# Kernel tuning notes

Hardware: AMD Instinct MI355X
Metric: run time of the kernel (lower is better)

## Reference

```python
import jax, jax.numpy as jnp
import numpy as np
from math import factorial as fact

L_MAX = 3
K = 128
N = 8192

# ---- Clebsch-Gordan coefficients (Racah formula, real for integer l) ----

def _cg_coeff(l1, m1, l2, m2, l3, m3):
    if m1 + m2 != m3:
        return 0.0
    pref = ((2 * l3 + 1) * fact(l3 + l1 - l2) * fact(l3 - l1 + l2)
            * fact(l1 + l2 - l3) / fact(l1 + l2 + l3 + 1)) ** 0.5
    pref *= (fact(l3 + m3) * fact(l3 - m3) * fact(l1 - m1) * fact(l1 + m1)
             * fact(l2 - m2) * fact(l2 + m2)) ** 0.5
    s = 0.0
    for k in range(max(0, l2 - l3 - m1, l1 - l3 + m2),
                   min(l1 + l2 - l3, l1 - m1, l2 + m2) + 1):
        s += (-1) ** k / (fact(k) * fact(l1 + l2 - l3 - k) * fact(l1 - m1 - k)
                          * fact(l2 + m2 - k) * fact(l3 - l2 + m1 + k)
                          * fact(l3 - l1 - m2 + k))
    return pref * s


def _cg_tensor(l1, l2, l3):
    C = np.zeros((2 * l1 + 1, 2 * l2 + 1, 2 * l3 + 1), dtype=np.float32)
    for m1 in range(-l1, l1 + 1):
        for m2 in range(-l2, l2 + 1):
            m3 = m1 + m2
            if -l3 <= m3 <= l3:
                C[m1 + l1, m2 + l2, m3 + l3] = _cg_coeff(l1, m1, l2, m2, l3, m3)
    return jnp.asarray(C)

# all allowed (l1, l2, l3) coupling paths, deterministic order
PATHS = [(l1, l2, l3)
         for l1 in range(L_MAX + 1)
         for l2 in range(L_MAX + 1)
         for l3 in range(abs(l1 - l2), min(l1 + l2, L_MAX) + 1)]
CG = {p: _cg_tensor(*p) for p in PATHS}
N_PATHS = [sum(1 for p in PATHS if p[2] == l3) for l3 in range(L_MAX + 1)]  # [4,9,11,10]


def setup_inputs() -> dict:
    key = jax.random.key(0)
    ks = jax.random.split(key, 12)
    inp = {}
    for i, l in enumerate(range(L_MAX + 1)):
        inp[f"f1_l{l}"] = jax.random.normal(ks[i], (N, 2 * l + 1, K), jnp.float32)
        inp[f"f2_l{l}"] = jax.random.normal(ks[4 + i], (N, 2 * l + 1, K), jnp.float32)
        fan_in = N_PATHS[l] * K
        inp[f"W_l{l}"] = jax.random.normal(ks[8 + i], (fan_in, K), jnp.float32) / np.sqrt(fan_in)
    return inp


def _forward(f1, f2, W):
    # CG tensor product: per-path contraction, channel-wise in k
    tp = [[] for _ in range(L_MAX + 1)]
    for (l1, l2, l3) in PATHS:
        C = CG[(l1, l2, l3)]  # [2l1+1, 2l2+1, 2l3+1]
        tp[l3].append(jnp.einsum('abm,nak,nbk->nmk', C, f1[l1], f2[l2]))
    # concat paths along channels, linear mix back to K, residual add
    outs = []
    for l3 in range(L_MAX + 1):
        cat = jnp.concatenate(tp[l3], axis=-1)        # [N, 2l3+1, n_paths*K]
        mixed = jnp.einsum('nmp,pk->nmk', cat, W[l3])  # [N, 2l3+1, K]
        outs.append(f1[l3] + mixed)
    return tuple(outs)


def reference(f1_l0, f1_l1, f1_l2, f1_l3,
              f2_l0, f2_l1, f2_l2, f2_l3,
              W_l0, W_l1, W_l2, W_l3):
    f1 = [f1_l0, f1_l1, f1_l2, f1_l3]
    f2 = [f2_l0, f2_l1, f2_l2, f2_l3]
    W = [W_l0, W_l1, W_l2, W_l3]
    return _forward(f1, f2, W)
```

## Files before the change

### kernel.cpp

```cpp
#include <hip/hip_runtime.h>

#define K_DIM 128

typedef __attribute__((ext_vector_type(8))) short short8;
typedef __attribute__((ext_vector_type(4))) float f32x4;

constexpr int C_L1[34] = {0,0,0,0, 1,1,1,1,1,1,1,1,1, 2,2,2,2,2,2,2,2,2,2,2, 3,3,3,3,3,3,3,3,3,3};
constexpr int C_L2[34] = {0,1,2,3, 0,1,1,1,2,2,2,3,3, 0,1,1,1,2,2,2,2,3,3,3, 0,1,1,2,2,2,3,3,3,3};
constexpr int C_L3[34] = {0,1,2,3, 1,0,1,2,1,2,3,2,3, 2,1,2,3,0,1,2,3,1,2,3, 3,2,3,1,2,3,0,1,2,3};
constexpr int C_NP[4]  = {4,9,11,10};
constexpr int C_PL[4][11] = {
  {0,5,17,30, 0,0,0,0,0,0,0},
  {1,4,6,8,14,18,21,27,31, 0,0},
  {2,7,9,11,13,15,19,22,25,28,32},
  {3,10,12,16,20,23,24,26,29,33, 0}
};
constexpr int C_CSUM[4] = {0,8,26,48};
constexpr size_t FOFF[4] = {0, 1048576, 4194304, 9437184};
constexpr int FSZ[4] = {1048576, 3145728, 5242880, 7340032};
constexpr size_t FTOT = 16777216;

__device__ double dfactd(int n){ double r=1.0; for(int i=2;i<=n;++i) r*=(double)i; return r; }

__device__ __forceinline__ unsigned short f2bf(float x) {
    unsigned int b = __float_as_uint(x);
    return (unsigned short)((b + 0x7FFFu + ((b >> 16) & 1u)) >> 16);
}
__device__ __forceinline__ float bflo(unsigned int u){ return __uint_as_float(u << 16); }
__device__ __forceinline__ float bfhi(unsigned int u){ return __uint_as_float(u & 0xFFFF0000u); }

__device__ __forceinline__ unsigned int cvtpk(float lo, float hi) {
    unsigned int r;
    asm("v_cvt_pk_bf16_f32 %0, %1, %2" : "=v"(r) : "v"(lo), "v"(hi));
    return r;
}

__global__ void cg_init(float* __restrict__ C2) {
    int e = blockIdx.x*blockDim.x + threadIdx.x;
    if (e >= 34*49) return;
    int p = e/49, r = e%49, m1i = r/7, m2i = r%7;
    int l1 = C_L1[p], l2 = C_L2[p], l3 = C_L3[p];
    float val = 0.f;
    if (m1i < 2*l1+1 && m2i < 2*l2+1) {
        int m1 = m1i-l1, m2 = m2i-l2, m3 = m1+m2;
        if (m3 >= -l3 && m3 <= l3) {
            double pref = sqrt((double)(2*l3+1) * dfactd(l3+l1-l2)*dfactd(l3-l1+l2)
                               * dfactd(l1+l2-l3) / dfactd(l1+l2+l3+1));
            pref *= sqrt(dfactd(l3+m3)*dfactd(l3-m3)*dfactd(l1-m1)*dfactd(l1+m1)
                         *dfactd(l2-m2)*dfactd(l2+m2));
            int kmin = max(0, max(l2-l3-m1, l1-l3+m2));
            int kmax = min(l1+l2-l3, min(l1-m1, l2+m2));
            double s = 0.0;
            for (int k=kmin;k<=kmax;++k) {
                double t = dfactd(k)*dfactd(l1+l2-l3-k)*dfactd(l1-m1-k)
                         * dfactd(l2+m2-k)*dfactd(l3-l2+m1+k)*dfactd(l3-l1-m2+k);
                s += ((k&1)? -1.0:1.0)/t;
            }
            val = (float)(pref*s);
        }
    }
    C2[e] = val;
}

__global__ void wt_prep(const float* __restrict__ W0, const float* __restrict__ W1,
                        const float* __restrict__ W2, const float* __restrict__ W3,
                        unsigned short* __restrict__ wt) {
    int b = blockIdx.x;
    int chunk = b >> 5;
    int e = ((b & 31) << 8) + threadIdx.x;
    int kk = e & 63, col = e >> 6;
    int l3 = (chunk < 8) ? 0 : (chunk < 26) ? 1 : (chunk < 48) ? 2 : 3;
    int local = chunk - C_CSUM[l3];
    int kin = local*64 + kk;
    const float* W = (l3==0)?W0:(l3==1)?W1:(l3==2)?W2:W3;
    float v = W[(size_t)kin*K_DIM + col];
    wt[(size_t)chunk*8192 + col*64 + (kk ^ ((col&7)<<3))] = f2bf(v);
}

__global__ void fpack(const float* __restrict__ s0, const float* __restrict__ s1,
                      const float* __restrict__ s2, const float* __restrict__ s3,
                      const float* __restrict__ s4, const float* __restrict__ s5,
                      const float* __restrict__ s6, const float* __restrict__ s7,
                      unsigned short* __restrict__ dst) {
    int y = blockIdx.y;
    int l = y & 3, fi = y >> 2;
    const float* srcs[8] = {s0,s1,s2,s3,s4,s5,s6,s7};
    const float* src = srcs[y];
    int i4 = blockIdx.x*256 + threadIdx.x;
    if (i4*4 >= FSZ[l]) return;
    float4 v = reinterpret_cast<const float4*>(src)[i4];
    unsigned int u0 = (unsigned int)f2bf(v.x) | ((unsigned int)f2bf(v.y) << 16);
    unsigned int u1 = (unsigned int)f2bf(v.z) | ((unsigned int)f2bf(v.w) << 16);
    unsigned short* d = dst + fi*FTOT + FOFF[l] + (size_t)i4*4;
    *reinterpret_cast<uint2*>(d) = make_uint2(u0, u1);
}

template<int L3, int PI>
__device__ __forceinline__ void res_path(
    const unsigned int (&q1)[16][2], const unsigned int (&q2)[16][2],
    const unsigned short* __restrict__ wt, const float* __restrict__ C2,
    float* C2s, unsigned char* Asb,
    int tid, int nodel, int chq, int wid, int lr, int lg, f32x4 (&cacc)[2*L3+1])
{
    constexpr int P  = C_PL[L3][PI];
    constexpr int l1 = C_L1[P], l2 = C_L2[P];
    constexpr int d1 = 2*l1+1, d2 = 2*l2+1;
    constexpr int TL3 = 2*L3+1;

    if (tid < 49) C2s[tid] = C2[P*49 + tid];
    __syncthreads();

    const int col = 16*wid + lr;
    const int wkey = (col&7)<<4;
    const unsigned char* wb0 = (const unsigned char*)(wt + (size_t)(C_CSUM[L3] + PI*2    )*8192);
    const unsigned char* wb1 = (const unsigned char*)(wt + (size_t)(C_CSUM[L3] + PI*2 + 1)*8192);
    short8 wf[4];
    wf[0] = *reinterpret_cast<const short8*>(wb0 + col*128 + ((16*lg     ) ^ wkey));
    wf[1] = *reinterpret_cast<const short8*>(wb0 + col*128 + ((16*lg + 64) ^ wkey));
    wf[2] = *reinterpret_cast<const short8*>(wb1 + col*128 + ((16*lg     ) ^ wkey));
    wf[3] = *reinterpret_cast<const short8*>(wb1 + col*128 + ((16*lg + 64) ^ wkey));

    #pragma unroll
    for (int h=0; h<2; ++h) {
        float a[TL3][2];
        #pragma unroll
        for (int mt=0; mt<TL3; ++mt) { a[mt][0]=0.f; a[mt][1]=0.f; }
        #pragma unroll
        for (int m2i=0; m2i<d2; ++m2i) {
            float y0 = bflo(q2[l2*l2+m2i][h]);
            float y1 = bfhi(q2[l2*l2+m2i][h]);
            #pragma unroll
            for (int m1i=0; m1i<d1; ++m1i) {
                int mt = (m1i-l1) + (m2i-l2) + L3;
                if (mt >= 0 && mt < TL3) {
                    float c = C2s[m1i*7 + m2i];
                    a[mt][0] = fmaf(c*bflo(q1[l1*l1+m1i][h]), y0, a[mt][0]);
                    a[mt][1] = fmaf(c*bfhi(q1[l1*l1+m1i][h]), y1, a[mt][1]);
                }
            }
        }
        #pragma unroll
        for (int mt=0; mt<TL3; ++mt) {
            int row = nodel*TL3 + mt;
            *reinterpret_cast<unsigned int*>(
                Asb + row*256 + h*128 + ((chq*4) ^ ((row&7)<<4))) = cvtpk(a[mt][0], a[mt][1]);
        }
    }
    __syncthreads();

    #pragma unroll
    for (int kst=0; kst<4; ++kst) {
        #pragma unroll
        for (int rt=0; rt<TL3; ++rt) {
            int arow = 16*rt + lr;
            short8 af = *reinterpret_cast<const short8*>(
                Asb + arow*256 + ((16*lg + 64*kst) ^ ((arow&7)<<4)));
            cacc[rt] = __builtin_amdgcn_mfma_f32_16x16x32_bf16(af, wf[kst], cacc[rt], 0, 0, 0);
        }
    }
}

template<int L3, int PI>
__device__ __forceinline__ void res_paths(
    const unsigned int (&q1)[16][2], const unsigned int (&q2)[16][2],
    const unsigned short* __restrict__ wt, const float* __restrict__ C2,
    float* C2s, unsigned char* Asb,
    int tid, int nodel, int chq, int wid, int lr, int lg, f32x4 (&cacc)[2*L3+1])
{
    if constexpr (PI < C_NP[L3]) {
        res_path<L3, PI>(q1, q2, wt, C2, C2s, Asb, tid, nodel, chq, wid, lr, lg, cacc);
        res_paths<L3, PI+1>(q1, q2, wt, C2, C2s, Asb, tid, nodel, chq, wid, lr, lg, cacc);
    }
}

template<int L3>
__device__ __forceinline__ void run16(
    int n0,
    const unsigned short* __restrict__ f1b, const unsigned short* __restrict__ f2b,
    const unsigned short* __restrict__ wt, const float* __restrict__ C2,
    float* __restrict__ out, float* C2s, unsigned char* Asb)
{
    constexpr int TL3 = 2*L3+1;
    const int tid   = threadIdx.x;
    const int nodel = tid >> 5;
    const int chq   = tid & 31;
    const int lane  = tid & 63, wid = tid >> 6;
    const int lr    = lane & 15, lg = lane >> 4;
    constexpr size_t OB = FOFF[L3];

    unsigned int q1[16][2], q2[16][2];
    #pragma unroll
    for (int l=0; l<4; ++l) {
        const unsigned short* g1 = f1b + FOFF[l] + (size_t)(n0+nodel)*((2*l+1)*128) + chq*2;
        const unsigned short* g2 = f2b + FOFF[l] + (size_t)(n0+nodel)*((2*l+1)*128) + chq*2;
        #pragma unroll
        for (int m=0; m<2*l+1; ++m) {
            #pragma unroll
            for (int h=0; h<2; ++h) {
                q1[l*l+m][h] = *reinterpret_cast<const unsigned int*>(g1 + m*128 + h*64);
                q2[l*l+m][h] = *reinterpret_cast<const unsigned int*>(g2 + m*128 + h*64);
            }
        }
    }

    f32x4 cacc[TL3];
    #pragma unroll
    for (int rt=0; rt<TL3; ++rt) cacc[rt] = (f32x4){0.f,0.f,0.f,0.f};

    res_paths<L3, 0>(q1, q2, wt, C2, C2s, Asb, tid, nodel, chq, wid, lr, lg, cacc);

    __syncthreads();
    float* S = reinterpret_cast<float*>(Asb);
    const unsigned short* __restrict__ fr = f1b + OB;
    const int col = 16*wid + lr;
    const int rr = tid >> 5, c0 = (tid & 31) * 4;
    #pragma unroll
    for (int rt=0; rt<TL3; ++rt) {
        #pragma unroll
        for (int i=0;i<4;++i)
            S[(4*lg+i)*128 + col] = cacc[rt][i];
        __syncthreads();
        {
            size_t ro = (size_t)(n0*TL3 + 16*rt + rr) * K_DIM;
            float4 v = *reinterpret_cast<const float4*>(&S[rr*128 + c0]);
            uint2 rb = *reinterpret_cast<const uint2*>(fr + ro + c0);
            v.x += bflo(rb.x); v.y += bfhi(rb.x);
            v.z += bflo(rb.y); v.w += bfhi(rb.y);
            *reinterpret_cast<float4*>(&out[OB + ro + c0]) = v;
        }
        __syncthreads();
    }
}

__global__ __launch_bounds__(512, 2) void cg_main(
    const unsigned short* __restrict__ f1b, const unsigned short* __restrict__ f2b,
    const unsigned short* __restrict__ wt,
    const float* __restrict__ C2, float* __restrict__ out)
{
    __shared__ __align__(16) unsigned char Asb[28672];
    __shared__ float C2s[49];

    int bid = blockIdx.x;
    int x = bid & 7, j = bid >> 3;
    int rnd = j >> 4, k = j & 15;
    int l3 = k >> 2, q = k & 3;
    int n0 = x*1024 + rnd*64 + q*16;
    if (l3 == 0)      run16<0>(n0, f1b, f2b, wt, C2, out, C2s, Asb);
    else if (l3 == 1) run16<1>(n0, f1b, f2b, wt, C2, out, C2s, Asb);
    else if (l3 == 2) run16<2>(n0, f1b, f2b, wt, C2, out, C2s, Asb);
    else              run16<3>(n0, f1b, f2b, wt, C2, out, C2s, Asb);
}

extern "C" void kernel_launch(void* const* d_in, const int* in_sizes, int n_in,
                              void* d_out, int out_size, void* d_ws, size_t ws_size,
                              hipStream_t stream) {
    const float* f10 = (const float*)d_in[0];
    const float* f20 = (const float*)d_in[1];
    const float* W0  = (const float*)d_in[2];
    const float* f11 = (const float*)d_in[3];
    const float* f21 = (const float*)d_in[4];
    const float* W1  = (const float*)d_in[5];
    const float* f12 = (const float*)d_in[6];
    const float* f22 = (const float*)d_in[7];
    const float* W2  = (const float*)d_in[8];
    const float* f13 = (const float*)d_in[9];
    const float* f23 = (const float*)d_in[10];
    const float* W3  = (const float*)d_in[11];

    float* C2 = (float*)d_ws;
    unsigned short* wtw = (unsigned short*)((char*)d_ws + 8192);
    unsigned short* f1b = (unsigned short*)((char*)d_ws + 1122304);
    unsigned short* f2b = f1b + FTOT;
    float* out = (float*)d_out;

    hipLaunchKernelGGL(cg_init, dim3(7), dim3(256), 0, stream, C2);
    hipLaunchKernelGGL(wt_prep, dim3(68*32), dim3(256), 0, stream, W0, W1, W2, W3, wtw);
    hipLaunchKernelGGL(fpack, dim3(7168, 8), dim3(256), 0, stream,
        f10, f11, f12, f13, f20, f21, f22, f23, f1b);
    hipLaunchKernelGGL(cg_main, dim3(2048), dim3(512), 0, stream,
        f1b, f2b, wtw, C2, out);
}
```

Before: 174.1 us.

## Double-buffer CG path staging to overlap tensor product with MFMA

The per-path loop now uses two LDS staging buffers and two CG coefficient slots. Each iteration computes the next path's tensor product into one buffer while MFMAs consume the other, with one barrier per path instead of two. The epilogue also writes up to four row tiles per barrier pair into a padded (stride 132) staging area to cut barriers and bank conflicts. Shared memory per block roughly doubles to about 57KB, which may limit the two-blocks-per-CU occupancy target.

```diff
diff --git a/kernel.cpp b/kernel.cpp
--- a/kernel.cpp
+++ b/kernel.cpp
@@ -96,35 +96,23 @@
 }
 
 template<int L3, int PI>
-__device__ __forceinline__ void res_path(
+__device__ __forceinline__ void tp_into(
     const unsigned int (&q1)[16][2], const unsigned int (&q2)[16][2],
-    const unsigned short* __restrict__ wt, const float* __restrict__ C2,
-    float* C2s, unsigned char* Asb,
-    int tid, int nodel, int chq, int wid, int lr, int lg, f32x4 (&cacc)[2*L3+1])
+    const float* __restrict__ C2slot, unsigned char* __restrict__ Ab,
+    int nodel, int chq)
 {
     constexpr int P  = C_PL[L3][PI];
     constexpr int l1 = C_L1[P], l2 = C_L2[P];
     constexpr int d1 = 2*l1+1, d2 = 2*l2+1;
     constexpr int TL3 = 2*L3+1;
-
-    if (tid < 49) C2s[tid] = C2[P*49 + tid];
-    __syncthreads();
-
-    const int col = 16*wid + lr;
-    const int wkey = (col&7)<<4;
-    const unsigned char* wb0 = (const unsigned char*)(wt + (size_t)(C_CSUM[L3] + PI*2    )*8192);
-    const unsigned char* wb1 = (const unsigned char*)(wt + (size_t)(C_CSUM[L3] + PI*2 + 1)*8192);
-    short8 wf[4];
-    wf[0] = *reinterpret_cast<const short8*>(wb0 + col*128 + ((16*lg     ) ^ wkey));
-    wf[1] = *reinterpret_cast<const short8*>(wb0 + col*128 + ((16*lg + 64) ^ wkey));
-    wf[2] = *reinterpret_cast<const short8*>(wb1 + col*128 + ((16*lg     ) ^ wkey));
-    wf[3] = *reinterpret_cast<const short8*>(wb1 + col*128 + ((16*lg + 64) ^ wkey));
-
     #pragma unroll
     for (int h=0; h<2; ++h) {
+        float xlo[d1], xhi[d1];
+        #pragma unroll
+        for (int m=0;m<d1;++m) { xlo[m]=bflo(q1[l1*l1+m][h]); xhi[m]=bfhi(q1[l1*l1+m][h]); }
         float a[TL3][2];
         #pragma unroll
-        for (int mt=0; mt<TL3; ++mt) { a[mt][0]=0.f; a[mt][1]=0.f; }
+        for (int mt=0;mt<TL3;++mt){ a[mt][0]=0.f; a[mt][1]=0.f; }
         #pragma unroll
         for (int m2i=0; m2i<d2; ++m2i) {
             float y0 = bflo(q2[l2*l2+m2i][h]);
@@ -133,9 +121,9 @@
             for (int m1i=0; m1i<d1; ++m1i) {
                 int mt = (m1i-l1) + (m2i-l2) + L3;
                 if (mt >= 0 && mt < TL3) {
-                    float c = C2s[m1i*7 + m2i];
-                    a[mt][0] = fmaf(c*bflo(q1[l1*l1+m1i][h]), y0, a[mt][0]);
-                    a[mt][1] = fmaf(c*bfhi(q1[l1*l1+m1i][h]), y1, a[mt][1]);
+                    float c = C2slot[m1i*7 + m2i];
+                    a[mt][0] = fmaf(c*xlo[m1i], y0, a[mt][0]);
+                    a[mt][1] = fmaf(c*xhi[m1i], y1, a[mt][1]);
                 }
             }
         }
@@ -143,34 +131,60 @@
         for (int mt=0; mt<TL3; ++mt) {
             int row = nodel*TL3 + mt;
             *reinterpret_cast<unsigned int*>(
-                Asb + row*256 + h*128 + ((chq*4) ^ ((row&7)<<4))) = cvtpk(a[mt][0], a[mt][1]);
-        }
-    }
-    __syncthreads();
-
+                Ab + row*256 + h*128 + ((chq*4) ^ ((row&7)<<4))) = cvtpk(a[mt][0], a[mt][1]);
+        }
+    }
+}
+
+template<int L3, int PI>
+__device__ __forceinline__ void load_wf(const unsigned short* __restrict__ wt,
+                                        int col, int lg, short8 (&wf)[4]) {
+    const int wkey = (col&7)<<4;
+    const unsigned char* wb0 = (const unsigned char*)(wt + (size_t)(C_CSUM[L3] + PI*2    )*8192);
+    const unsigned char* wb1 = (const unsigned char*)(wt + (size_t)(C_CSUM[L3] + PI*2 + 1)*8192);
+    wf[0] = *reinterpret_cast<const short8*>(wb0 + col*128 + ((16*lg     ) ^ wkey));
+    wf[1] = *reinterpret_cast<const short8*>(wb0 + col*128 + ((16*lg + 64) ^ wkey));
+    wf[2] = *reinterpret_cast<const short8*>(wb1 + col*128 + ((16*lg     ) ^ wkey));
+    wf[3] = *reinterpret_cast<const short8*>(wb1 + col*128 + ((16*lg + 64) ^ wkey));
+}
+
+template<int L3>
+__device__ __forceinline__ void mfma_from(
+    const unsigned char* __restrict__ Ab, const short8 (&wf)[4],
+    int lr, int lg, f32x4 (&cacc)[2*L3+1])
+{
+    constexpr int TL3 = 2*L3+1;
     #pragma unroll
     for (int kst=0; kst<4; ++kst) {
         #pragma unroll
         for (int rt=0; rt<TL3; ++rt) {
             int arow = 16*rt + lr;
             short8 af = *reinterpret_cast<const short8*>(
-                Asb + arow*256 + ((16*lg + 64*kst) ^ ((arow&7)<<4)));
+                Ab + arow*256 + ((16*lg + 64*kst) ^ ((arow&7)<<4)));
             cacc[rt] = __builtin_amdgcn_mfma_f32_16x16x32_bf16(af, wf[kst], cacc[rt], 0, 0, 0);
         }
     }
 }
 
 template<int L3, int PI>
-__device__ __forceinline__ void res_paths(
+__device__ __forceinline__ void pipe(
     const unsigned int (&q1)[16][2], const unsigned int (&q2)[16][2],
     const unsigned short* __restrict__ wt, const float* __restrict__ C2,
-    float* C2s, unsigned char* Asb,
-    int tid, int nodel, int chq, int wid, int lr, int lg, f32x4 (&cacc)[2*L3+1])
-{
-    if constexpr (PI < C_NP[L3]) {
-        res_path<L3, PI>(q1, q2, wt, C2, C2s, Asb, tid, nodel, chq, wid, lr, lg, cacc);
-        res_paths<L3, PI+1>(q1, q2, wt, C2, C2s, Asb, tid, nodel, chq, wid, lr, lg, cacc);
-    }
+    float (&C2s)[2][49], unsigned char* A0, unsigned char* A1,
+    int tid, int nodel, int chq, int col, int lr, int lg, f32x4 (&cacc)[2*L3+1])
+{
+    constexpr int NP = C_NP[L3];
+    short8 wf[4];
+    load_wf<L3, PI>(wt, col, lg, wf);
+    if constexpr (PI+2 < NP) {
+        if (tid < 49) C2s[PI&1][tid] = C2[C_PL[L3][PI+2]*49 + tid];
+    }
+    if constexpr (PI+1 < NP)
+        tp_into<L3, PI+1>(q1, q2, C2s[(PI+1)&1], ((PI+1)&1) ? A1 : A0, nodel, chq);
+    mfma_from<L3>((PI&1) ? A1 : A0, wf, lr, lg, cacc);
+    __syncthreads();
+    if constexpr (PI+1 < NP)
+        pipe<L3, PI+1>(q1, q2, wt, C2, C2s, A0, A1, tid, nodel, chq, col, lr, lg, cacc);
 }
 
 template<int L3>
@@ -178,15 +192,19 @@
     int n0,
     const unsigned short* __restrict__ f1b, const unsigned short* __restrict__ f2b,
     const unsigned short* __restrict__ wt, const float* __restrict__ C2,
-    float* __restrict__ out, float* C2s, unsigned char* Asb)
+    float* __restrict__ out, float (&C2s)[2][49], unsigned char* Asb)
 {
     constexpr int TL3 = 2*L3+1;
+    constexpr int NP  = C_NP[L3];
     const int tid   = threadIdx.x;
     const int nodel = tid >> 5;
     const int chq   = tid & 31;
     const int lane  = tid & 63, wid = tid >> 6;
     const int lr    = lane & 15, lg = lane >> 4;
+    const int col   = 16*wid + lr;
     constexpr size_t OB = FOFF[L3];
+    unsigned char* A0 = Asb;
+    unsigned char* A1 = Asb + 28672;
 
     unsigned int q1[16][2], q2[16][2];
     #pragma unroll
@@ -207,26 +225,42 @@
     #pragma unroll
     for (int rt=0; rt<TL3; ++rt) cacc[rt] = (f32x4){0.f,0.f,0.f,0.f};
 
-    res_paths<L3, 0>(q1, q2, wt, C2, C2s, Asb, tid, nodel, chq, wid, lr, lg, cacc);
-
+    if (tid < 49) {
+        C2s[0][tid] = C2[C_PL[L3][0]*49 + tid];
+        if constexpr (NP > 1) C2s[1][tid] = C2[C_PL[L3][1]*49 + tid];
+    }
     __syncthreads();
+    tp_into<L3, 0>(q1, q2, C2s[0], A0, nodel, chq);
+    __syncthreads();
+    pipe<L3, 0>(q1, q2, wt, C2, C2s, A0, A1, tid, nodel, chq, col, lr, lg, cacc);
+
     float* S = reinterpret_cast<float*>(Asb);
     const unsigned short* __restrict__ fr = f1b + OB;
-    const int col = 16*wid + lr;
-    const int rr = tid >> 5, c0 = (tid & 31) * 4;
-    #pragma unroll
-    for (int rt=0; rt<TL3; ++rt) {
-        #pragma unroll
-        for (int i=0;i<4;++i)
-            S[(4*lg+i)*128 + col] = cacc[rt][i];
+    #pragma unroll
+    for (int rt0=0; rt0<TL3; rt0+=4) {
+        const int bn = (TL3 - rt0 < 4) ? (TL3 - rt0) : 4;
+        #pragma unroll
+        for (int rtl=0; rtl<4; ++rtl) {
+            if (rtl < bn) {
+                #pragma unroll
+                for (int i=0;i<4;++i)
+                    S[(rtl*16 + 4*lg + i)*132 + col] = cacc[rt0+rtl][i];
+            }
+        }
         __syncthreads();
-        {
-            size_t ro = (size_t)(n0*TL3 + 16*rt + rr) * K_DIM;
-            float4 v = *reinterpret_cast<const float4*>(&S[rr*128 + c0]);
-            uint2 rb = *reinterpret_cast<const uint2*>(fr + ro + c0);
-            v.x += bflo(rb.x); v.y += bfhi(rb.x);
-            v.z += bflo(rb.y); v.w += bfhi(rb.y);
-            *reinterpret_cast<float4*>(&out[OB + ro + c0]) = v;
+        #pragma unroll
+        for (int it=0; it<4; ++it) {
+            if (it < bn) {
+                int s = tid + it*512;
+                int rows = s >> 5, cq = (s & 31) * 4;
+                int gr = n0*TL3 + (rt0 + (rows >> 4))*16 + (rows & 15);
+                size_t ro = (size_t)gr * K_DIM;
+                float4 v = *reinterpret_cast<const float4*>(&S[rows*132 + cq]);
+                uint2 rb = *reinterpret_cast<const uint2*>(fr + ro + cq);
+                v.x += bflo(rb.x); v.y += bfhi(rb.x);
+                v.z += bflo(rb.y); v.w += bfhi(rb.y);
+                *reinterpret_cast<float4*>(&out[OB + ro + cq]) = v;
+            }
         }
         __syncthreads();
     }
@@ -237,8 +271,8 @@
     const unsigned short* __restrict__ wt,
     const float* __restrict__ C2, float* __restrict__ out)
 {
-    __shared__ __align__(16) unsigned char Asb[28672];
-    __shared__ float C2s[49];
+    __shared__ __align__(16) unsigned char Asb[2*28672];
+    __shared__ float C2s[2][49];
 
     int bid = blockIdx.x;
     int x = bid & 7, j = bid >> 3;
```

After: 159.6 us. -8.4%, faster.
